# Kernel optimization log

Hardware: AMD Instinct MI355X
Metric: run time of the kernel (lower is better)

## Reference

```python
import jax, jax.numpy as jnp
import numpy as np

B, T, D, H = 2, 4096, 512, 8
HD = D // H

def setup_inputs() -> dict:
    key = jax.random.key(0)
    ks = jax.random.split(key, 5)
    x = jax.random.normal(ks[0], (B, T, D), dtype=jnp.float32)
    # causal mask: masked_fill where mask == 0
    mask = jnp.tril(jnp.ones((T, T), dtype=jnp.int32))[None, None, :, :]
    qkv_w = jax.random.normal(ks[1], (D, 3 * D), dtype=jnp.float32) * (D ** -0.5)
    qkv_b = jax.random.normal(ks[2], (3 * D,), dtype=jnp.float32) * 0.02
    proj_w = jax.random.normal(ks[3], (D, D), dtype=jnp.float32) * (D ** -0.5)
    proj_b = jax.random.normal(ks[4], (D,), dtype=jnp.float32) * 0.02
    return {"x": x, "mask": mask, "qkv_w": qkv_w, "qkv_b": qkv_b,
            "proj_w": proj_w, "proj_b": proj_b}

def reference(x, mask, qkv_w, qkv_b, proj_w, proj_b):
    b, t, c = x.shape
    qkv = x @ qkv_w + qkv_b                      # [B,T,3D]
    q, k, v = jnp.split(qkv, 3, axis=-1)
    # [B,T,D] -> [B,H,T,hd]
    def heads(a):
        return a.reshape(b, t, H, HD).transpose(0, 2, 1, 3)
    q, k, v = heads(q), heads(k), heads(v)
    att = jnp.einsum('bhqd,bhkd->bhqk', q, k) / (HD ** 0.5)
    att = jnp.where(mask == 0, -jnp.inf, att)
    att = jax.nn.softmax(att, axis=-1)           # dropout p=0.0 -> identity
    out = jnp.einsum('bhqk,bhkd->bhqd', att, v)  # [B,H,T,hd]
    out = out.transpose(0, 2, 1, 3).reshape(b, t, c)
    return out @ proj_w + proj_b
```

## Files before the change

### kernel.cpp

```cpp
#include <hip/hip_runtime.h>
#include <hip/hip_bf16.h>


typedef __attribute__((ext_vector_type(8))) short bf16x8;
typedef __attribute__((ext_vector_type(4))) float f32x4;
typedef __attribute__((ext_vector_type(16))) float f32x16;
typedef __attribute__((ext_vector_type(2))) int i32x2;

#define DEV static __device__ __forceinline__

DEV unsigned short f2bf(float f) {
    union { float f; unsigned u; } a; a.f = f;
    unsigned r = a.u + 0x7FFFu + ((a.u >> 16) & 1u);
    return (unsigned short)(r >> 16);
}

DEV unsigned pack2(float a, float b) {
    unsigned r;
    asm("v_cvt_pk_bf16_f32 %0, %1, %2" : "=v"(r) : "v"(a), "v"(b));
    return r;
}

DEV void glds16(const void* g, void* l) {
    __builtin_amdgcn_global_load_lds(
        (const __attribute__((address_space(1))) void*)g,
        (__attribute__((address_space(3))) void*)l,
        16, 0, 0);
}

DEV f32x4 mfma(bf16x8 a, bf16x8 b, f32x4 c) {
    return __builtin_amdgcn_mfma_f32_16x16x32_bf16(a, b, c, 0, 0, 0);
}

DEV f32x16 mfma32(bf16x8 a, bf16x8 b, f32x16 c) {
    return __builtin_amdgcn_mfma_f32_32x32x16_bf16(a, b, c, 0, 0, 0);
}

DEV void plswap(unsigned& a, unsigned& b) {
#if __has_builtin(__builtin_amdgcn_permlane32_swap)
    i32x2 r = __builtin_amdgcn_permlane32_swap((int)a, (int)b, false, false);
    a = (unsigned)r.x; b = (unsigned)r.y;
#else
    unsigned sa = __shfl_xor(a, 32), sb = __shfl_xor(b, 32);
    bool hi = (threadIdx.x & 32) != 0;
    unsigned na = hi ? sb : a;
    unsigned nb = hi ? b : sa;
    a = na; b = nb;
#endif
}

DEV float xhalf_sum(float x) {
    unsigned a = __float_as_uint(x), b = a;
    plswap(a, b);
    return __uint_as_float(a) + __uint_as_float(b);
}

__global__ __launch_bounds__(256) void k_prep(const float* __restrict__ x,
                                              unsigned short* __restrict__ xb,
                                              const float* __restrict__ qkv_w,
                                              unsigned short* __restrict__ wqkvT,
                                              const float* __restrict__ proj_w,
                                              unsigned short* __restrict__ wprojT) {
    const int tid = threadIdx.x;
    int id = blockIdx.x;
    if (id < 2048) {
        const int n4 = 8192 * 512 / 4;
        for (int i = id * 256 + tid; i < n4; i += 2048 * 256) {
            float4 v = ((const float4*)x)[i];
            ushort4 o;
            o.x = f2bf(v.x); o.y = f2bf(v.y); o.z = f2bf(v.z); o.w = f2bf(v.w);
            ((ushort4*)xb)[i] = o;
        }
        return;
    }
    id -= 2048;
    __shared__ float t[64][65];
    const float* src; unsigned short* dst; int R, C, bx, by;
    if (id < 192) { src = qkv_w; dst = wqkvT; R = 512; C = 1536; bx = id % 24; by = id / 24; }
    else { id -= 192; src = proj_w; dst = wprojT; R = 512; C = 512; bx = id & 7; by = id >> 3; }
#pragma unroll
    for (int e = 0; e < 16; ++e) {
        int idx = e * 256 + tid;
        int r = idx >> 6, c = idx & 63;
        t[r][c] = src[(by * 64 + r) * C + bx * 64 + c];
    }
    __syncthreads();
#pragma unroll
    for (int e = 0; e < 16; ++e) {
        int idx = e * 256 + tid;
        int r = idx >> 6, c = idx & 63;
        dst[(bx * 64 + r) * R + by * 64 + c] = f2bf(t[c][r]);
    }
}

__global__ __launch_bounds__(256) void k_gemm_qkv(
    const unsigned short* __restrict__ xb, const unsigned short* __restrict__ wT,
    const float* __restrict__ bias,
    unsigned short* __restrict__ Qb, unsigned short* __restrict__ Kb,
    unsigned short* __restrict__ Vtb)
{
    __shared__ __attribute__((aligned(16))) unsigned short lA[128 * 64];
    __shared__ __attribute__((aligned(16))) unsigned short lB[128 * 64];
    const int tid = threadIdx.x, lane = tid & 63, w = tid >> 6;
    const int qi = lane & 15, g = lane >> 4;
    const int bm = blockIdx.x & 63, bn = blockIdx.x >> 6;
    const int m0 = bm * 128, n0 = bn * 128;
    const int wr = w >> 1, wc = w & 1;
    const int srow = lane >> 3, sch = (lane & 7) ^ srow;
    const int swz = (qi & 7) << 4;
    f32x4 zero = {0.f, 0.f, 0.f, 0.f};
    f32x4 acc[4][4];
#pragma unroll
    for (int i = 0; i < 4; ++i)
#pragma unroll
        for (int j = 0; j < 4; ++j) acc[i][j] = zero;

    for (int kt = 0; kt < 8; ++kt) {
#pragma unroll
        for (int i = 0; i < 4; ++i) {
            int c = w * 4 + i;
            int row = c * 8 + srow;
            glds16(xb + (m0 + row) * 512 + kt * 64 + sch * 8, (char*)lA + c * 1024);
            glds16(wT + (n0 + row) * 512 + kt * 64 + sch * 8, (char*)lB + c * 1024);
        }
        __syncthreads();
#pragma unroll
        for (int k2 = 0; k2 < 2; ++k2) {
            bf16x8 af[4], bfr[4];
#pragma unroll
            for (int i = 0; i < 4; ++i) {
                int ra = wr * 64 + i * 16 + qi;
                af[i] = *(const bf16x8*)((const char*)lA + ra * 128 + ((k2 * 64 + g * 16) ^ swz));
                int rb = wc * 64 + i * 16 + qi;
                bfr[i] = *(const bf16x8*)((const char*)lB + rb * 128 + ((k2 * 64 + g * 16) ^ swz));
            }
#pragma unroll
            for (int mi = 0; mi < 4; ++mi)
#pragma unroll
                for (int ni = 0; ni < 4; ++ni)
                    acc[mi][ni] = mfma(af[mi], bfr[ni], acc[mi][ni]);
        }
        __syncthreads();
    }

    const int comp = n0 >> 9;
#pragma unroll
    for (int mi = 0; mi < 4; ++mi) {
        int mbase = m0 + wr * 64 + mi * 16 + g * 4;
        int b = mbase >> 12, t = mbase & 4095;
#pragma unroll
        for (int ni = 0; ni < 4; ++ni) {
            int n = n0 + wc * 64 + ni * 16 + qi;
            float bn = bias[n];
            int nn = n & 511;
            int h = nn >> 6, d = nn & 63;
            if (comp == 0) {
                unsigned short* dst = Qb + ((b * 8 + h) * 4096 + t) * 64 + d;
#pragma unroll
                for (int r = 0; r < 4; ++r)
                    dst[r * 64] = f2bf((acc[mi][ni][r] + bn) * 0.18033688011112042f);
            } else if (comp == 1) {
                unsigned short* dst = Kb + ((b * 8 + h) * 4096 + t) * 64 + d;
#pragma unroll
                for (int r = 0; r < 4; ++r)
                    dst[r * 64] = f2bf(acc[mi][ni][r] + bn);
            } else {
                ushort4 pk4;
                pk4.x = f2bf(acc[mi][ni][0] + bn);
                pk4.y = f2bf(acc[mi][ni][1] + bn);
                pk4.z = f2bf(acc[mi][ni][2] + bn);
                pk4.w = f2bf(acc[mi][ni][3] + bn);
                *(ushort4*)(Vtb + ((b * 8 + h) * 64 + d) * 4096 + t) = pk4;
            }
        }
    }
}

__global__ __launch_bounds__(512) void k_attn(
    const unsigned short* __restrict__ Qb, const unsigned short* __restrict__ Kb,
    const unsigned short* __restrict__ Vtb, unsigned short* __restrict__ Ob)
{
    __shared__ __attribute__((aligned(16))) char smem[65536];
    const int tid = threadIdx.x, lane = tid & 63, w = tid >> 6;
    const int l31 = lane & 31, l7 = lane & 7, h = lane >> 5;
    const int pr = w >> 1, sub = w & 1;
    const int idx = blockIdx.x;
    const int bh = idx & 15;
    const int p = idx >> 4;
    const unsigned short* Qh = Qb + bh * 4096 * 64;
    const unsigned short* Kh = Kb + bh * 4096 * 64;
    const unsigned short* Vh = Vtb + bh * 4096 * 64;
    const float NEGINF = -__builtin_inff();

    char* myK = smem + pr * 16384;
    char* myV = myK + 8192;

    const int srw = lane >> 3;
    const int sxor = (l7 ^ srw) * 8;
    const int kOffE = (sub * 32 + srw) * 64 + sxor;
    const int vOffE = (sub * 32 + srw) * 4096 + sxor;
    const int ldsO = sub * 4096;

    const int rowbase = l31 * 128;
    int cx[4];
#pragma unroll
    for (int c = 0; c < 4; ++c) cx[c] = ((2 * c + h) ^ l7) * 16;

    const int qrel = (sub << 5) + l31;

    f32x16 z16;
#pragma unroll
    for (int r = 0; r < 16; ++r) z16[r] = 0.f;

    for (int si = 0; si < 2; ++si) {
        const int qt = si ? p : 63 - p;
        const int Tmax = (qt >> 2) + 1;
        const int qrow = qt * 64 + sub * 32 + l31;

        bf16x8 qf[4];
#pragma unroll
        for (int c = 0; c < 4; ++c)
            qf[c] = *(const bf16x8*)(Qh + qrow * 64 + 16 * c + 8 * h);

        f32x16 o0 = z16, o1 = z16;
        float li = 0.f;

        for (int t = 0; t < Tmax; ++t) {
            const int j = 4 * t + pr;
            const bool act = (j <= qt);
            if (act) {
                const unsigned short* kp = Kh + j * 4096 + kOffE;
                const unsigned short* vp = Vh + vOffE + j * 64;
#pragma unroll
                for (int i = 0; i < 4; ++i) {
                    glds16(kp + i * 512,   myK + ldsO + i * 1024);
                    glds16(vp + i * 32768, myV + ldsO + i * 1024);
                }
            }
            __syncthreads();
            if (act) {
                const char* lk = myK;
                const char* lv = myV;
                f32x16 s0, s1;
                __builtin_amdgcn_s_setprio(1);
                {
                    bf16x8 k0 = *(const bf16x8*)(lk + rowbase + cx[0]);
                    bf16x8 k1 = *(const bf16x8*)(lk + 4096 + rowbase + cx[0]);
                    s0 = mfma32(k0, qf[0], z16);
                    s1 = mfma32(k1, qf[0], z16);
                }
#pragma unroll
                for (int c = 1; c < 4; ++c) {
                    bf16x8 k0 = *(const bf16x8*)(lk + rowbase + cx[c]);
                    bf16x8 k1 = *(const bf16x8*)(lk + 4096 + rowbase + cx[c]);
                    s0 = mfma32(k0, qf[c], s0);
                    s1 = mfma32(k1, qf[c], s1);
                }
                __builtin_amdgcn_s_setprio(0);

                if (j == qt) {
#pragma unroll
                    for (int r = 0; r < 16; ++r) {
                        int rr = 4 * h + (r & 3) + 8 * (r >> 2);
                        if (rr > qrel) s0[r] = NEGINF;
                        if (rr + 32 > qrel) s1[r] = NEGINF;
                    }
                }

#pragma unroll
                for (int r = 0; r < 16; ++r) {
                    s0[r] = __builtin_amdgcn_exp2f(s0[r]);
                    s1[r] = __builtin_amdgcn_exp2f(s1[r]);
                }
                float a8[8];
#pragma unroll
                for (int r = 0; r < 8; ++r)
                    a8[r] = (s0[r] + s0[r + 8]) + (s1[r] + s1[r + 8]);
                float b0 = (a8[0] + a8[4]) + (a8[1] + a8[5]);
                float b1 = (a8[2] + a8[6]) + (a8[3] + a8[7]);
                li += xhalf_sum(b0 + b1);

                __builtin_amdgcn_s_setprio(1);
#pragma unroll
                for (int c2 = 0; c2 < 4; ++c2) {
                    unsigned u0w, u1w, u2w, u3w;
                    if (c2 < 2) {
                        const int b0i = 8 * c2;
                        u0w = pack2(s0[b0i + 0], s0[b0i + 1]);
                        u1w = pack2(s0[b0i + 2], s0[b0i + 3]);
                        u2w = pack2(s0[b0i + 4], s0[b0i + 5]);
                        u3w = pack2(s0[b0i + 6], s0[b0i + 7]);
                    } else {
                        const int b0i = 8 * (c2 - 2);
                        u0w = pack2(s1[b0i + 0], s1[b0i + 1]);
                        u1w = pack2(s1[b0i + 2], s1[b0i + 3]);
                        u2w = pack2(s1[b0i + 4], s1[b0i + 5]);
                        u3w = pack2(s1[b0i + 6], s1[b0i + 7]);
                    }
                    plswap(u0w, u2w);
                    plswap(u1w, u3w);
                    union { unsigned u[4]; bf16x8 v; } pf;
                    pf.u[0] = u0w; pf.u[1] = u1w; pf.u[2] = u2w; pf.u[3] = u3w;
                    bf16x8 v0 = *(const bf16x8*)(lv + rowbase + cx[c2]);
                    bf16x8 v1 = *(const bf16x8*)(lv + 4096 + rowbase + cx[c2]);
                    o0 = mfma32(v0, pf.v, o0);
                    o1 = mfma32(v1, pf.v, o1);
                }
                __builtin_amdgcn_s_setprio(0);
            }
            __syncthreads();
        }

        float* fsm = (float*)smem;
        if (pr != 0) {
            float* slot = fsm + ((((pr - 1) << 1) + sub) * 64 + lane) * 36;
#pragma unroll
            for (int r4 = 0; r4 < 4; ++r4) {
                f32x4 v0 = {o0[4 * r4], o0[4 * r4 + 1], o0[4 * r4 + 2], o0[4 * r4 + 3]};
                f32x4 v1 = {o1[4 * r4], o1[4 * r4 + 1], o1[4 * r4 + 2], o1[4 * r4 + 3]};
                *(f32x4*)(slot + 4 * r4) = v0;
                *(f32x4*)(slot + 16 + 4 * r4) = v1;
            }
            slot[32] = li;
        }
        __syncthreads();
        if (pr == 0) {
            float l = li;
#pragma unroll
            for (int i = 0; i < 3; ++i) {
                const float* s = fsm + (((i << 1) + sub) * 64 + lane) * 36;
                l += s[32];
#pragma unroll
                for (int r4 = 0; r4 < 4; ++r4) {
                    f32x4 a = *(const f32x4*)(s + 4 * r4);
                    f32x4 b = *(const f32x4*)(s + 16 + 4 * r4);
#pragma unroll
                    for (int e = 0; e < 4; ++e) {
                        o0[4 * r4 + e] += a[e];
                        o1[4 * r4 + e] += b[e];
                    }
                }
            }
            float inv = 1.f / l;
            unsigned short* orow = Ob + ((bh >> 3) * 4096 + qrow) * 512 + (bh & 7) * 64 + 4 * h;
#pragma unroll
            for (int g2 = 0; g2 < 4; ++g2) {
                union { ushort4 s4; unsigned u[2]; } a;
                a.u[0] = pack2(o0[4 * g2 + 0] * inv, o0[4 * g2 + 1] * inv);
                a.u[1] = pack2(o0[4 * g2 + 2] * inv, o0[4 * g2 + 3] * inv);
                *(ushort4*)(orow + 8 * g2) = a.s4;
                a.u[0] = pack2(o1[4 * g2 + 0] * inv, o1[4 * g2 + 1] * inv);
                a.u[1] = pack2(o1[4 * g2 + 2] * inv, o1[4 * g2 + 3] * inv);
                *(ushort4*)(orow + 32 + 8 * g2) = a.s4;
            }
        }
        __syncthreads();
    }
}

__global__ __launch_bounds__(256) void k_gemm_proj(
    const unsigned short* __restrict__ Ob, const unsigned short* __restrict__ wT,
    const float* __restrict__ bias, float* __restrict__ out)
{
    __shared__ __attribute__((aligned(16))) char ls[32768];
    unsigned short* lA = (unsigned short*)ls;
    unsigned short* lB = (unsigned short*)(ls + 16384);
    const int tid = threadIdx.x, lane = tid & 63, w = tid >> 6;
    const int qi = lane & 15, g = lane >> 4;
    const int bm = blockIdx.x & 63, bn = blockIdx.x >> 6;
    const int m0 = bm * 128, n0 = bn * 128;
    const int wr = w >> 1, wc = w & 1;
    const int srow = lane >> 3, sch = (lane & 7) ^ srow;
    const int swz = (qi & 7) << 4;
    f32x4 zero = {0.f, 0.f, 0.f, 0.f};
    f32x4 acc[4][4];
#pragma unroll
    for (int i = 0; i < 4; ++i)
#pragma unroll
        for (int j = 0; j < 4; ++j) acc[i][j] = zero;

    for (int kt = 0; kt < 8; ++kt) {
#pragma unroll
        for (int i = 0; i < 4; ++i) {
            int c = w * 4 + i;
            int row = c * 8 + srow;
            glds16(Ob + (m0 + row) * 512 + kt * 64 + sch * 8, (char*)lA + c * 1024);
            glds16(wT + (n0 + row) * 512 + kt * 64 + sch * 8, (char*)lB + c * 1024);
        }
        __syncthreads();
#pragma unroll
        for (int k2 = 0; k2 < 2; ++k2) {
            bf16x8 af[4], bfr[4];
#pragma unroll
            for (int i = 0; i < 4; ++i) {
                int ra = wr * 64 + i * 16 + qi;
                af[i] = *(const bf16x8*)((const char*)lA + ra * 128 + ((k2 * 64 + g * 16) ^ swz));
                int rb = wc * 64 + i * 16 + qi;
                bfr[i] = *(const bf16x8*)((const char*)lB + rb * 128 + ((k2 * 64 + g * 16) ^ swz));
            }
#pragma unroll
            for (int mi = 0; mi < 4; ++mi)
#pragma unroll
                for (int ni = 0; ni < 4; ++ni)
                    acc[mi][ni] = mfma(af[mi], bfr[ni], acc[mi][ni]);
        }
        __syncthreads();
    }

    float bn4[4];
#pragma unroll
    for (int ni = 0; ni < 4; ++ni) bn4[ni] = bias[n0 + wc * 64 + ni * 16 + qi];

    float* st = (float*)ls;
#pragma unroll
    for (int cc = 0; cc < 4; ++cc) {
        __syncthreads();
        if (wr == (cc >> 1)) {
            const int mi0 = (cc & 1) * 2;
#pragma unroll
            for (int mm = 0; mm < 2; ++mm) {
                int mi = mi0 + mm;
                int rr0 = mi * 16 + g * 4 - (cc & 1) * 32;
#pragma unroll
                for (int ni = 0; ni < 4; ++ni) {
                    int col = wc * 64 + ni * 16 + qi;
#pragma unroll
                    for (int r = 0; r < 4; ++r)
                        st[(rr0 + r) * 132 + col] = acc[mi][ni][r] + bn4[ni];
                }
            }
        }
        __syncthreads();
#pragma unroll
        for (int e = 0; e < 4; ++e) {
            int fid = e * 256 + tid;
            int row = fid >> 5, c4 = fid & 31;
            f32x4 v = *(const f32x4*)(st + row * 132 + 4 * c4);
            *(f32x4*)(out + (m0 + cc * 32 + row) * 512 + n0 + 4 * c4) = v;
        }
    }
}

extern "C" void kernel_launch(void* const* d_in, const int* in_sizes, int n_in,
                              void* d_out, int out_size, void* d_ws, size_t ws_size,
                              hipStream_t stream) {
    const float* x      = (const float*)d_in[0];
    const float* qkv_w  = (const float*)d_in[2];
    const float* qkv_b  = (const float*)d_in[3];
    const float* proj_w = (const float*)d_in[4];
    const float* proj_b = (const float*)d_in[5];

    char* ws = (char*)d_ws;
    unsigned short* xb     = (unsigned short*)(ws);
    unsigned short* wqkvT  = (unsigned short*)(ws +  8388608);
    unsigned short* wprojT = (unsigned short*)(ws +  9961472);
    unsigned short* Qb     = (unsigned short*)(ws + 10485760);
    unsigned short* Kb     = (unsigned short*)(ws + 18874368);
    unsigned short* Vtb    = (unsigned short*)(ws + 27262976);
    unsigned short* Ob     = (unsigned short*)(ws + 35651584);
    float* out = (float*)d_out;

    k_prep<<<2304, 256, 0, stream>>>(x, xb, qkv_w, wqkvT, proj_w, wprojT);
    k_gemm_qkv<<<768, 256, 0, stream>>>(xb, wqkvT, qkv_b, Qb, Kb, Vtb);
    k_attn<<<512, 512, 0, stream>>>(Qb, Kb, Vtb, Ob);
    k_gemm_proj<<<256, 256, 0, stream>>>(Ob, wprojT, proj_b, out);
}
```

Measured before the change: 100.8 us.

## Double-buffer LDS tiles in QKV and projection GEMMs to overlap loads

```diff
diff --git a/kernel.cpp b/kernel.cpp
--- a/kernel.cpp
+++ b/kernel.cpp
@@ -99,8 +99,9 @@
     unsigned short* __restrict__ Qb, unsigned short* __restrict__ Kb,
     unsigned short* __restrict__ Vtb)
 {
-    __shared__ __attribute__((aligned(16))) unsigned short lA[128 * 64];
-    __shared__ __attribute__((aligned(16))) unsigned short lB[128 * 64];
+    __shared__ __attribute__((aligned(16))) char smem[65536];
+    char* lA0 = smem;          char* lB0 = smem + 16384;
+    char* lA1 = smem + 32768;  char* lB1 = smem + 49152;
     const int tid = threadIdx.x, lane = tid & 63, w = tid >> 6;
     const int qi = lane & 15, g = lane >> 4;
     const int bm = blockIdx.x & 63, bn = blockIdx.x >> 6;
@@ -115,24 +116,44 @@
 #pragma unroll
         for (int j = 0; j < 4; ++j) acc[i][j] = zero;
 
+#pragma unroll
+    for (int i = 0; i < 4; ++i) {
+        int c = w * 4 + i;
+        int row = c * 8 + srow;
+        glds16(xb + (m0 + row) * 512 + sch * 8, lA0 + c * 1024);
+        glds16(wT + (n0 + row) * 512 + sch * 8, lB0 + c * 1024);
+    }
+
     for (int kt = 0; kt < 8; ++kt) {
-#pragma unroll
-        for (int i = 0; i < 4; ++i) {
-            int c = w * 4 + i;
-            int row = c * 8 + srow;
-            glds16(xb + (m0 + row) * 512 + kt * 64 + sch * 8, (char*)lA + c * 1024);
-            glds16(wT + (n0 + row) * 512 + kt * 64 + sch * 8, (char*)lB + c * 1024);
-        }
-        __syncthreads();
+        const int cur = kt & 1;
+        if (kt + 1 < 8) {
+            char* ad = cur ? lA0 : lA1;
+            char* bd = cur ? lB0 : lB1;
+#pragma unroll
+            for (int i = 0; i < 4; ++i) {
+                int c = w * 4 + i;
+                int row = c * 8 + srow;
+                glds16(xb + (m0 + row) * 512 + (kt + 1) * 64 + sch * 8, ad + c * 1024);
+                glds16(wT + (n0 + row) * 512 + (kt + 1) * 64 + sch * 8, bd + c * 1024);
+            }
+            asm volatile("s_waitcnt vmcnt(8)" ::: "memory");
+        } else {
+            asm volatile("s_waitcnt vmcnt(0)" ::: "memory");
+        }
+        __builtin_amdgcn_s_barrier();
+        __builtin_amdgcn_sched_barrier(0);
+
+        const char* la = cur ? lA1 : lA0;
+        const char* lb = cur ? lB1 : lB0;
 #pragma unroll
         for (int k2 = 0; k2 < 2; ++k2) {
             bf16x8 af[4], bfr[4];
 #pragma unroll
             for (int i = 0; i < 4; ++i) {
                 int ra = wr * 64 + i * 16 + qi;
-                af[i] = *(const bf16x8*)((const char*)lA + ra * 128 + ((k2 * 64 + g * 16) ^ swz));
+                af[i] = *(const bf16x8*)(la + ra * 128 + ((k2 * 64 + g * 16) ^ swz));
                 int rb = wc * 64 + i * 16 + qi;
-                bfr[i] = *(const bf16x8*)((const char*)lB + rb * 128 + ((k2 * 64 + g * 16) ^ swz));
+                bfr[i] = *(const bf16x8*)(lb + rb * 128 + ((k2 * 64 + g * 16) ^ swz));
             }
 #pragma unroll
             for (int mi = 0; mi < 4; ++mi)
@@ -140,7 +161,8 @@
                 for (int ni = 0; ni < 4; ++ni)
                     acc[mi][ni] = mfma(af[mi], bfr[ni], acc[mi][ni]);
         }
-        __syncthreads();
+        __builtin_amdgcn_s_barrier();
+        __builtin_amdgcn_sched_barrier(0);
     }
 
     const int comp = n0 >> 9;
@@ -362,9 +384,9 @@
     const unsigned short* __restrict__ Ob, const unsigned short* __restrict__ wT,
     const float* __restrict__ bias, float* __restrict__ out)
 {
-    __shared__ __attribute__((aligned(16))) char ls[32768];
-    unsigned short* lA = (unsigned short*)ls;
-    unsigned short* lB = (unsigned short*)(ls + 16384);
+    __shared__ __attribute__((aligned(16))) char smem[65536];
+    char* lA0 = smem;          char* lB0 = smem + 16384;
+    char* lA1 = smem + 32768;  char* lB1 = smem + 49152;
     const int tid = threadIdx.x, lane = tid & 63, w = tid >> 6;
     const int qi = lane & 15, g = lane >> 4;
     const int bm = blockIdx.x & 63, bn = blockIdx.x >> 6;
@@ -379,24 +401,44 @@
 #pragma unroll
         for (int j = 0; j < 4; ++j) acc[i][j] = zero;
 
+#pragma unroll
+    for (int i = 0; i < 4; ++i) {
+        int c = w * 4 + i;
+        int row = c * 8 + srow;
+        glds16(Ob + (m0 + row) * 512 + sch * 8, lA0 + c * 1024);
+        glds16(wT + (n0 + row) * 512 + sch * 8, lB0 + c * 1024);
+    }
+
     for (int kt = 0; kt < 8; ++kt) {
-#pragma unroll
-        for (int i = 0; i < 4; ++i) {
-            int c = w * 4 + i;
-            int row = c * 8 + srow;
-            glds16(Ob + (m0 + row) * 512 + kt * 64 + sch * 8, (char*)lA + c * 1024);
-            glds16(wT + (n0 + row) * 512 + kt * 64 + sch * 8, (char*)lB + c * 1024);
-        }
-        __syncthreads();
+        const int cur = kt & 1;
+        if (kt + 1 < 8) {
+            char* ad = cur ? lA0 : lA1;
+            char* bd = cur ? lB0 : lB1;
+#pragma unroll
+            for (int i = 0; i < 4; ++i) {
+                int c = w * 4 + i;
+                int row = c * 8 + srow;
+                glds16(Ob + (m0 + row) * 512 + (kt + 1) * 64 + sch * 8, ad + c * 1024);
+                glds16(wT + (n0 + row) * 512 + (kt + 1) * 64 + sch * 8, bd + c * 1024);
+            }
+            asm volatile("s_waitcnt vmcnt(8)" ::: "memory");
+        } else {
+            asm volatile("s_waitcnt vmcnt(0)" ::: "memory");
+        }
+        __builtin_amdgcn_s_barrier();
+        __builtin_amdgcn_sched_barrier(0);
+
+        const char* la = cur ? lA1 : lA0;
+        const char* lb = cur ? lB1 : lB0;
 #pragma unroll
         for (int k2 = 0; k2 < 2; ++k2) {
             bf16x8 af[4], bfr[4];
 #pragma unroll
             for (int i = 0; i < 4; ++i) {
                 int ra = wr * 64 + i * 16 + qi;
-                af[i] = *(const bf16x8*)((const char*)lA + ra * 128 + ((k2 * 64 + g * 16) ^ swz));
+                af[i] = *(const bf16x8*)(la + ra * 128 + ((k2 * 64 + g * 16) ^ swz));
                 int rb = wc * 64 + i * 16 + qi;
-                bfr[i] = *(const bf16x8*)((const char*)lB + rb * 128 + ((k2 * 64 + g * 16) ^ swz));
+                bfr[i] = *(const bf16x8*)(lb + rb * 128 + ((k2 * 64 + g * 16) ^ swz));
             }
 #pragma unroll
             for (int mi = 0; mi < 4; ++mi)
@@ -404,14 +446,15 @@
                 for (int ni = 0; ni < 4; ++ni)
                     acc[mi][ni] = mfma(af[mi], bfr[ni], acc[mi][ni]);
         }
-        __syncthreads();
+        __builtin_amdgcn_s_barrier();
+        __builtin_amdgcn_sched_barrier(0);
     }
 
     float bn4[4];
 #pragma unroll
     for (int ni = 0; ni < 4; ++ni) bn4[ni] = bias[n0 + wc * 64 + ni * 16 + qi];
 
-    float* st = (float*)ls;
+    float* st = (float*)smem;
 #pragma unroll
     for (int cc = 0; cc < 4; ++cc) {
         __syncthreads();
```

Result: faster. 93.48 us, median of 3 (-7.2%).
